# Kernel optimization log

Hardware: AMD Instinct MI355X
Metric: run time of the kernel (lower is better)

## Reference

```python
import jax, jax.numpy as jnp
import numpy as np

N_QUBITS = 6
DIM = 2 ** N_QUBITS  # 64


def _b(t, nd):
    # broadcast a (B,) per-sample angle factor (or scalar) against a state slice of rank nd
    if jnp.ndim(t) == 0:
        return t
    return t.reshape((t.shape[0],) + (1,) * (nd - 1))


def _ry(state, theta, q):
    ax = q + 1
    s0 = jnp.take(state, 0, axis=ax)
    s1 = jnp.take(state, 1, axis=ax)
    h = theta * 0.5
    c = _b(jnp.cos(h), s0.ndim)
    s = _b(jnp.sin(h), s0.ndim)
    return jnp.stack([c * s0 - s * s1, s * s0 + c * s1], axis=ax)


def _rx(state, theta, q):
    ax = q + 1
    s0 = jnp.take(state, 0, axis=ax)
    s1 = jnp.take(state, 1, axis=ax)
    h = theta * 0.5
    c = _b(jnp.cos(h), s0.ndim)
    s = _b(jnp.sin(h), s0.ndim)
    return jnp.stack([c * s0 - 1j * s * s1, -1j * s * s0 + c * s1], axis=ax)


def _rz(state, theta, q):
    ax = q + 1
    s0 = jnp.take(state, 0, axis=ax)
    s1 = jnp.take(state, 1, axis=ax)
    h = theta * 0.5
    p0 = _b(jnp.exp(-1j * h), s0.ndim)
    p1 = _b(jnp.exp(1j * h), s0.ndim)
    return jnp.stack([p0 * s0, p1 * s1], axis=ax)


def _cnot(state, ctrl, tgt):
    ca = ctrl + 1
    s0 = jnp.take(state, 0, axis=ca)
    s1 = jnp.take(state, 1, axis=ca)
    ta = tgt + 1 if tgt < ctrl else tgt  # target axis after removing control axis
    s1 = jnp.flip(s1, axis=ta)
    return jnp.stack([s0, s1], axis=ca)


def quantum_circuit(inputs, weights):
    # inputs: (B, 6) float; weights: (5, 6) float -> (B, 6) PauliZ expectations
    B = inputs.shape[0]
    scaled = jnp.clip(inputs, -1.0, 1.0) * jnp.pi
    state = jnp.zeros((B,) + (2,) * N_QUBITS, dtype=jnp.complex64)
    state = state.at[(slice(None),) + (0,) * N_QUBITS].set(1.0)
    for i in range(N_QUBITS):
        state = _ry(state, scaled[:, i], i)
    for i in range(N_QUBITS):
        state = _rx(state, weights[0, i], i)
        state = _rz(state, weights[1, i], i)
    for i in range(N_QUBITS - 1):
        state = _cnot(state, i, i + 1)
    state = _cnot(state, N_QUBITS - 1, 0)
    for i in range(N_QUBITS):
        state = _ry(state, weights[2, i], i)
        state = _rz(state, weights[3, i], i)
    for i in range(0, N_QUBITS, 2):
        state = _cnot(state, i, (i + 1) % N_QUBITS)
    for i in range(N_QUBITS):
        state = _rx(state, weights[4, i], i)
    probs = (state.real ** 2 + state.imag ** 2).reshape(B, DIM)
    # Z eigenvalue table: qubit q is bit (5-q) of the flat index
    k = jnp.arange(DIM)
    z = (1 - 2 * ((k[None, :] >> (N_QUBITS - 1 - jnp.arange(N_QUBITS)[:, None])) & 1)).astype(jnp.float32)
    return probs @ z.T  # (B, 6)


def setup_inputs() -> dict:
    key = jax.random.key(0)
    ks = jax.random.split(key, 13)
    B, n_symptoms, n_dep, nq = 262144, 128, 20, N_QUBITS

    def lin(k, fi, fo):
        bound = 1.0 / np.sqrt(fi)
        kw, kb = jax.random.split(k)
        W = jax.random.uniform(kw, (fi, fo), jnp.float32, -bound, bound)
        b = jax.random.uniform(kb, (fo,), jnp.float32, -bound, bound)
        return W, b

    x = jax.random.normal(ks[0], (B, n_symptoms), jnp.float32)
    W1, b1 = lin(ks[1], n_symptoms, 32)
    W2, b2 = lin(ks[2], 32, 16)
    W3, b3 = lin(ks[3], 16, nq)
    qw = jax.random.normal(ks[4], (5, nq), jnp.float32)
    W4, b4 = lin(ks[5], nq, 16)
    W5, b5 = lin(ks[6], 16, n_dep)
    return {"x": x, "W1": W1, "b1": b1, "W2": W2, "b2": b2, "W3": W3, "b3": b3,
            "qw": qw, "W4": W4, "b4": b4, "W5": W5, "b5": b5}


def reference(x, W1, b1, W2, b2, W3, b3, qw, W4, b4, W5, b5):
    h = jax.nn.relu(x @ W1 + b1)            # Dropout(0.2) is identity at eval
    h = jax.nn.relu(h @ W2 + b2)
    pre = jnp.tanh(h @ W3 + b3)             # (B, 6)
    # Original detaches before the quantum circuit -> stop_gradient for fidelity
    q_out = quantum_circuit(jax.lax.stop_gradient(pre), jax.lax.stop_gradient(qw))
    h = jax.nn.relu(q_out @ W4 + b4)
    return h @ W5 + b5                      # (B, n_departments)
```

## Files before the change

### kernel.cpp

```cpp
#include <hip/hip_runtime.h>
#include <hip/hip_bf16.h>
#include <math.h>

#define PI_F 3.14159265358979323846f

typedef float f32x4 __attribute__((ext_vector_type(4)));
typedef short bf16x8 __attribute__((ext_vector_type(8)));

__device__ __forceinline__ unsigned short bf_hi(float f) {
    return (unsigned short)(__float_as_uint(f) >> 16);
}
__device__ __forceinline__ float from_bf(unsigned short h) {
    return __uint_as_float(((unsigned)h) << 16);
}

__global__ __launch_bounds__(64) void build_u(const float* __restrict__ qw,
                                              float* __restrict__ Umat) {
    const int l = threadIdx.x;
    const int b = blockIdx.x;

    float ar = (l == b) ? 1.0f : 0.0f;
    float ai = 0.0f;

    #pragma unroll
    for (int i = 0; i < 6; ++i) {
        const int mask = 1 << (5 - i);
        float th = 0.5f * qw[0 * 6 + i];
        float c = cosf(th), sn = sinf(th);
        float pr = __shfl_xor(ar, mask);
        float pi = __shfl_xor(ai, mask);
        float nr = c * ar + sn * pi;
        float ni = c * ai - sn * pr;
        ar = nr; ai = ni;
        th = 0.5f * qw[1 * 6 + i];
        c = cosf(th); sn = sinf(th);
        float zn = (l & mask) ? 1.0f : -1.0f;
        nr = c * ar - zn * sn * ai;
        ni = c * ai + zn * sn * ar;
        ar = nr; ai = ni;
    }

    #pragma unroll
    for (int i = 0; i < 6; ++i) {
        const int ctrl = i, tgt = (i + 1) % 6;
        const int cm = 1 << (5 - ctrl), tm = 1 << (5 - tgt);
        float pr = __shfl_xor(ar, tm);
        float pi = __shfl_xor(ai, tm);
        bool take = (l & cm) != 0;
        ar = take ? pr : ar;
        ai = take ? pi : ai;
    }

    #pragma unroll
    for (int i = 0; i < 6; ++i) {
        const int mask = 1 << (5 - i);
        float th = 0.5f * qw[2 * 6 + i];
        float c = cosf(th), sn = sinf(th);
        float pr = __shfl_xor(ar, mask);
        float pi = __shfl_xor(ai, mask);
        float sg = (l & mask) ? sn : -sn;
        float nr = c * ar + sg * pr;
        float ni = c * ai + sg * pi;
        ar = nr; ai = ni;
        th = 0.5f * qw[3 * 6 + i];
        c = cosf(th); sn = sinf(th);
        float zn = (l & mask) ? 1.0f : -1.0f;
        nr = c * ar - zn * sn * ai;
        ni = c * ai + zn * sn * ar;
        ar = nr; ai = ni;
    }

    #pragma unroll
    for (int i = 0; i < 6; i += 2) {
        const int cm = 1 << (5 - i), tm = 1 << (5 - (i + 1));
        float pr = __shfl_xor(ar, tm);
        float pi = __shfl_xor(ai, tm);
        bool take = (l & cm) != 0;
        ar = take ? pr : ar;
        ai = take ? pi : ai;
    }

    #pragma unroll
    for (int i = 0; i < 6; ++i) {
        const int mask = 1 << (5 - i);
        float th = 0.5f * qw[4 * 6 + i];
        float c = cosf(th), sn = sinf(th);
        float pr = __shfl_xor(ar, mask);
        float pi = __shfl_xor(ai, mask);
        float nr = c * ar + sn * pi;
        float ni = c * ai - sn * pr;
        ar = nr; ai = ni;
    }

    Umat[(l * 64 + b) * 2 + 0] = ar;
    Umat[(l * 64 + b) * 2 + 1] = ai;
}

__global__ __launch_bounds__(64) void convert_u(const float* __restrict__ Umat,
                                                unsigned short* __restrict__ Ubf) {
    const int l = threadIdx.x;
    bf16x8* out8 = reinterpret_cast<bf16x8*>(Ubf);

    #pragma unroll
    for (int ri = 0; ri < 2; ++ri) {
        #pragma unroll
        for (int t = 0; t < 4; ++t) {
            #pragma unroll
            for (int h = 0; h < 2; ++h) {
                const int vf = (ri * 4 + t) * 2 + h;
                bf16x8 vh, vl;
                #pragma unroll
                for (int e = 0; e < 8; ++e) {
                    const int k = 16 * t + (l & 15);
                    const int j = h * 32 + (l >> 4) * 8 + e;
                    float v = Umat[k * 128 + j * 2 + ri];
                    unsigned short hh = bf_hi(v);
                    float rem = v - from_bf(hh);
                    unsigned short ll = bf_hi(rem);
                    vh[e] = (short)hh;
                    vl[e] = (short)ll;
                }
                out8[(vf * 2 + 0) * 64 + l] = vh;
                out8[(vf * 2 + 1) * 64 + l] = vl;
            }
        }
    }
}

__device__ __forceinline__ void front_tail(
    const float h1[32],
    const float* __restrict__ W2, const float* __restrict__ b2,
    const float* __restrict__ W3, const float* __restrict__ b3,
    float lo[8], float hi[8])
{
    float h2[16];
    #pragma unroll
    for (int o = 0; o < 16; ++o) h2[o] = b2[o];
    #pragma unroll
    for (int j = 0; j < 32; ++j) {
        #pragma unroll
        for (int o = 0; o < 16; ++o) h2[o] = fmaf(h1[j], W2[j * 16 + o], h2[o]);
    }
    #pragma unroll
    for (int o = 0; o < 16; ++o) h2[o] = fmaxf(h2[o], 0.0f);

    float cq[6], sq[6];
    #pragma unroll
    for (int q = 0; q < 6; ++q) {
        float t = b3[q];
        #pragma unroll
        for (int j = 0; j < 16; ++j) t = fmaf(h2[j], W3[j * 6 + q], t);
        t = tanhf(t);
        t = fminf(1.0f, fmaxf(-1.0f, t));
        float half = t * (0.5f * PI_F);
        sq[q] = sinf(half);
        cq[q] = cosf(half);
    }

    {
        float f3[2] = {cq[3], sq[3]};
        float f4[2] = {cq[4], sq[4]};
        float f5[2] = {cq[5], sq[5]};
        #pragma unroll
        for (int m = 0; m < 8; ++m)
            lo[m] = f3[(m >> 2) & 1] * f4[(m >> 1) & 1] * f5[m & 1];
        float f0[2] = {cq[0], sq[0]};
        float f1[2] = {cq[1], sq[1]};
        float f2[2] = {cq[2], sq[2]};
        #pragma unroll
        for (int m = 0; m < 8; ++m)
            hi[m] = f0[(m >> 2) & 1] * f1[(m >> 1) & 1] * f2[m & 1];
    }
}

__global__ __launch_bounds__(256) void front_kernel(
    const float* __restrict__ x,
    const float* __restrict__ W1, const float* __restrict__ b1,
    const float* __restrict__ W2, const float* __restrict__ b2,
    const float* __restrict__ W3, const float* __restrict__ b3,
    float* __restrict__ tab, int B)
{
    __shared__ float Ls[256 * 36];

    const int tid = threadIdx.x;
    const long sbase = (long)blockIdx.x * 256;
    const int s = (int)(sbase + tid);

    const f32x4* xg = reinterpret_cast<const f32x4*>(x);

    float h1[32];
    #pragma unroll
    for (int o = 0; o < 32; ++o) h1[o] = b1[o];

    #pragma unroll 1
    for (int tile = 0; tile < 4; ++tile) {
        #pragma unroll
        for (int i = 0; i < 8; ++i) {
            const int flat = i * 256 + tid;
            const int row = flat >> 3;
            const int c4  = flat & 7;
            long srow = sbase + row;
            if (srow >= B) srow = B - 1;
            f32x4 v = __builtin_nontemporal_load(&xg[(size_t)srow * 32 + tile * 8 + c4]);
            *reinterpret_cast<f32x4*>(&Ls[row * 36 + c4 * 4]) = v;
        }
        __syncthreads();

        #pragma unroll
        for (int c4 = 0; c4 < 8; ++c4) {
            float4 xv = *reinterpret_cast<const float4*>(&Ls[tid * 36 + c4 * 4]);
            const float* w = W1 + (tile * 32 + c4 * 4) * 32;
            #pragma unroll
            for (int o = 0; o < 32; ++o) h1[o] = fmaf(xv.x, w[o], h1[o]);
            #pragma unroll
            for (int o = 0; o < 32; ++o) h1[o] = fmaf(xv.y, w[32 + o], h1[o]);
            #pragma unroll
            for (int o = 0; o < 32; ++o) h1[o] = fmaf(xv.z, w[64 + o], h1[o]);
            #pragma unroll
            for (int o = 0; o < 32; ++o) h1[o] = fmaf(xv.w, w[96 + o], h1[o]);
        }
        __syncthreads();
    }

    #pragma unroll
    for (int o = 0; o < 32; ++o) h1[o] = fmaxf(h1[o], 0.0f);

    float lo[8], hi[8];
    front_tail(h1, W2, b2, W3, b3, lo, hi);

    if (s < B) {
        #pragma unroll
        for (int i = 0; i < 8; ++i)
            __builtin_nontemporal_store(lo[i], &tab[(size_t)i * B + s]);
        #pragma unroll
        for (int i = 0; i < 8; ++i)
            __builtin_nontemporal_store(hi[i], &tab[(size_t)(8 + i) * B + s]);
    }
}

__global__ __launch_bounds__(256) void gemv_mfma(
    const float* __restrict__ tab,
    const unsigned short* __restrict__ Ubf,
    const float* __restrict__ W4, const float* __restrict__ b4,
    const float* __restrict__ W5, const float* __restrict__ b5,
    float* __restrict__ out, int B)
{
    __shared__ float qlds[64][8];

    const int tid  = threadIdx.x;
    const int wv   = tid >> 6;
    const int lane = tid & 63;
    const int g    = lane >> 4;
    const int c    = lane & 15;
    const long blk = (long)blockIdx.x * 64;
    const int s    = (int)(blk + wv * 16 + c);
    const int s_ld = (s < B) ? s : (B - 1);

    float tl[8], th[8];
    #pragma unroll
    for (int i = 0; i < 8; ++i)
        tl[i] = __builtin_nontemporal_load(&tab[(size_t)i * B + s_ld]);
    #pragma unroll
    for (int i = 0; i < 8; ++i)
        th[i] = __builtin_nontemporal_load(&tab[(size_t)(8 + i) * B + s_ld]);

    float bh0 = (g == 0) ? th[0] : (g == 1) ? th[1] : (g == 2) ? th[2] : th[3];
    float bh1 = (g == 0) ? th[4] : (g == 1) ? th[5] : (g == 2) ? th[6] : th[7];

    bf16x8 Ah0, Al0, Ah1, Al1;
    #pragma unroll
    for (int e = 0; e < 8; ++e) {
        float p0 = bh0 * tl[e];
        unsigned short h0 = bf_hi(p0);
        Ah0[e] = (short)h0;
        Al0[e] = (short)bf_hi(p0 - from_bf(h0));
        float p1 = bh1 * tl[e];
        unsigned short h1 = bf_hi(p1);
        Ah1[e] = (short)h1;
        Al1[e] = (short)bf_hi(p1 - from_bf(h1));
    }

    const bf16x8* Ub = reinterpret_cast<const bf16x8*>(Ubf);

    f32x4 accre[4], accim[4];
    #pragma unroll
    for (int t = 0; t < 4; ++t) { accre[t] = (f32x4)0.0f; accim[t] = (f32x4)0.0f; }

    #pragma unroll
    for (int t = 0; t < 4; ++t) {
        bf16x8 B0h = Ub[(((0 * 4 + t) * 2 + 0) * 2 + 0) * 64 + lane];
        bf16x8 B0l = Ub[(((0 * 4 + t) * 2 + 0) * 2 + 1) * 64 + lane];
        bf16x8 B1h = Ub[(((0 * 4 + t) * 2 + 1) * 2 + 0) * 64 + lane];
        bf16x8 B1l = Ub[(((0 * 4 + t) * 2 + 1) * 2 + 1) * 64 + lane];
        accre[t] = __builtin_amdgcn_mfma_f32_16x16x32_bf16(Ah0, B0h, accre[t], 0, 0, 0);
        accre[t] = __builtin_amdgcn_mfma_f32_16x16x32_bf16(Al0, B0h, accre[t], 0, 0, 0);
        accre[t] = __builtin_amdgcn_mfma_f32_16x16x32_bf16(Ah0, B0l, accre[t], 0, 0, 0);
        accre[t] = __builtin_amdgcn_mfma_f32_16x16x32_bf16(Ah1, B1h, accre[t], 0, 0, 0);
        accre[t] = __builtin_amdgcn_mfma_f32_16x16x32_bf16(Al1, B1h, accre[t], 0, 0, 0);
        accre[t] = __builtin_amdgcn_mfma_f32_16x16x32_bf16(Ah1, B1l, accre[t], 0, 0, 0);
    }
    #pragma unroll
    for (int t = 0; t < 4; ++t) {
        bf16x8 B0h = Ub[(((1 * 4 + t) * 2 + 0) * 2 + 0) * 64 + lane];
        bf16x8 B0l = Ub[(((1 * 4 + t) * 2 + 0) * 2 + 1) * 64 + lane];
        bf16x8 B1h = Ub[(((1 * 4 + t) * 2 + 1) * 2 + 0) * 64 + lane];
        bf16x8 B1l = Ub[(((1 * 4 + t) * 2 + 1) * 2 + 1) * 64 + lane];
        accim[t] = __builtin_amdgcn_mfma_f32_16x16x32_bf16(Ah0, B0h, accim[t], 0, 0, 0);
        accim[t] = __builtin_amdgcn_mfma_f32_16x16x32_bf16(Al0, B0h, accim[t], 0, 0, 0);
        accim[t] = __builtin_amdgcn_mfma_f32_16x16x32_bf16(Ah0, B0l, accim[t], 0, 0, 0);
        accim[t] = __builtin_amdgcn_mfma_f32_16x16x32_bf16(Ah1, B1h, accim[t], 0, 0, 0);
        accim[t] = __builtin_amdgcn_mfma_f32_16x16x32_bf16(Al1, B1h, accim[t], 0, 0, 0);
        accim[t] = __builtin_amdgcn_mfma_f32_16x16x32_bf16(Ah1, B1l, accim[t], 0, 0, 0);
    }

    #pragma unroll
    for (int r = 0; r < 4; ++r) {
        float p0 = accre[0][r] * accre[0][r] + accim[0][r] * accim[0][r];
        float p1 = accre[1][r] * accre[1][r] + accim[1][r] * accim[1][r];
        float p2 = accre[2][r] * accre[2][r] + accim[2][r] * accim[2][r];
        float p3 = accre[3][r] * accre[3][r] + accim[3][r] * accim[3][r];

        float P0 = p0 + p1 + p2 + p3;
        float P1 = p0 + p1 - p2 - p3;
        float P2 = p0 - p1 + p2 - p3;

        float v = P0;
        #pragma unroll
        for (int st = 0; st < 4; ++st) {
            const int m = 1 << st;
            float prt = __shfl_xor(v, m);
            v = (lane & m) ? (prt - v) : (prt + v);
        }
        #pragma unroll
        for (int st = 0; st < 4; ++st) P1 += __shfl_xor(P1, 1 << st);
        #pragma unroll
        for (int st = 0; st < 4; ++st) P2 += __shfl_xor(P2, 1 << st);

        const int sl = wv * 16 + g * 4 + r;
        if (c == 0) { qlds[sl][0] = P1; qlds[sl][1] = P2; }
        if (c == 8) qlds[sl][2] = v;
        if (c == 4) qlds[sl][3] = v;
        if (c == 2) qlds[sl][4] = v;
        if (c == 1) qlds[sl][5] = v;
    }

    __syncthreads();

    if (tid < 64) {
        const int so = (int)(blk + tid);
        if (so < B) {
            float qv[6];
            #pragma unroll
            for (int i = 0; i < 6; ++i) qv[i] = qlds[tid][i];

            float h4[16];
            #pragma unroll
            for (int o = 0; o < 16; ++o) h4[o] = b4[o];
            #pragma unroll
            for (int q = 0; q < 6; ++q) {
                #pragma unroll
                for (int o = 0; o < 16; ++o) h4[o] = fmaf(qv[q], W4[q * 16 + o], h4[o]);
            }
            #pragma unroll
            for (int o = 0; o < 16; ++o) h4[o] = fmaxf(h4[o], 0.0f);

            float o5[20];
            #pragma unroll
            for (int o = 0; o < 20; ++o) {
                float t = b5[o];
                #pragma unroll
                for (int j = 0; j < 16; ++j) t = fmaf(h4[j], W5[j * 20 + o], t);
                o5[o] = t;
            }

            f32x4* outv = reinterpret_cast<f32x4*>(out + (size_t)so * 20);
            #pragma unroll
            for (int i = 0; i < 5; ++i) {
                f32x4 v = {o5[4 * i], o5[4 * i + 1], o5[4 * i + 2], o5[4 * i + 3]};
                __builtin_nontemporal_store(v, &outv[i]);
            }
        }
    }
}

extern "C" void kernel_launch(void* const* d_in, const int* in_sizes, int n_in,
                              void* d_out, int out_size, void* d_ws, size_t ws_size,
                              hipStream_t stream) {
    const float* x  = (const float*)d_in[0];
    const float* W1 = (const float*)d_in[1];
    const float* b1 = (const float*)d_in[2];
    const float* W2 = (const float*)d_in[3];
    const float* b2 = (const float*)d_in[4];
    const float* W3 = (const float*)d_in[5];
    const float* b3 = (const float*)d_in[6];
    const float* qw = (const float*)d_in[7];
    const float* W4 = (const float*)d_in[8];
    const float* b4 = (const float*)d_in[9];
    const float* W5 = (const float*)d_in[10];
    const float* b5 = (const float*)d_in[11];
    float* out = (float*)d_out;

    const int B = in_sizes[0] / 128;

    float* Umat = (float*)d_ws;
    unsigned short* Ubf = (unsigned short*)((float*)d_ws + 8192);
    float* tab  = (float*)d_ws + 16384;

    build_u<<<64, 64, 0, stream>>>(qw, Umat);
    convert_u<<<1, 64, 0, stream>>>(Umat, Ubf);
    front_kernel<<<(B + 255) / 256, 256, 0, stream>>>(
        x, W1, b1, W2, b2, W3, b3, tab, B);
    gemv_mfma<<<(B + 63) / 64, 256, 0, stream>>>(
        tab, Ubf, W4, b4, W5, b5, out, B);
}
```

Measured before the change: 106.5 us.

## Move first MLP layer onto bf16x3 split MFMA with pre-split weights

The first linear layer (128->32) in the front kernel moves from per-thread scalar FMAs to MFMA 16x16x32 bf16 instructions. Inputs and W1 are split into high and low bf16 parts, and three products are accumulated to approximate fp32 precision. W1 is pre-split once in the merged conversion kernel. Results go through LDS so each thread can run the rest of the MLP on its sample. This cuts VALU FMA work and weight reloads, at the cost of a slight precision change, an extra LDS round trip, and uncoalesced per-row global loads of x.

```diff
diff --git a/kernel.cpp b/kernel.cpp
--- a/kernel.cpp
+++ b/kernel.cpp
@@ -96,8 +96,10 @@
     Umat[(l * 64 + b) * 2 + 1] = ai;
 }
 
-__global__ __launch_bounds__(64) void convert_u(const float* __restrict__ Umat,
-                                                unsigned short* __restrict__ Ubf) {
+__global__ __launch_bounds__(64) void convert_all(
+    const float* __restrict__ Umat, const float* __restrict__ W1,
+    unsigned short* __restrict__ Ubf, unsigned short* __restrict__ W1bf)
+{
     const int l = threadIdx.x;
     bf16x8* out8 = reinterpret_cast<bf16x8*>(Ubf);
 
@@ -115,14 +117,30 @@
                     const int j = h * 32 + (l >> 4) * 8 + e;
                     float v = Umat[k * 128 + j * 2 + ri];
                     unsigned short hh = bf_hi(v);
-                    float rem = v - from_bf(hh);
-                    unsigned short ll = bf_hi(rem);
                     vh[e] = (short)hh;
-                    vl[e] = (short)ll;
+                    vl[e] = (short)bf_hi(v - from_bf(hh));
                 }
                 out8[(vf * 2 + 0) * 64 + l] = vh;
                 out8[(vf * 2 + 1) * 64 + l] = vl;
             }
+        }
+    }
+
+    bf16x8* w8 = reinterpret_cast<bf16x8*>(W1bf);
+    #pragma unroll
+    for (int ks = 0; ks < 4; ++ks) {
+        #pragma unroll
+        for (int nt = 0; nt < 2; ++nt) {
+            bf16x8 vh, vl;
+            #pragma unroll
+            for (int e = 0; e < 8; ++e) {
+                float v = W1[(ks * 32 + (l >> 4) * 8 + e) * 32 + nt * 16 + (l & 15)];
+                unsigned short hh = bf_hi(v);
+                vh[e] = (short)hh;
+                vl[e] = (short)bf_hi(v - from_bf(hh));
+            }
+            w8[((ks * 2 + nt) * 2 + 0) * 64 + l] = vh;
+            w8[((ks * 2 + nt) * 2 + 1) * 64 + l] = vl;
         }
     }
 }
@@ -173,57 +191,78 @@
     }
 }
 
-__global__ __launch_bounds__(256) void front_kernel(
+__global__ __launch_bounds__(256) void front_mfma(
     const float* __restrict__ x,
-    const float* __restrict__ W1, const float* __restrict__ b1,
+    const unsigned short* __restrict__ W1bf, const float* __restrict__ b1,
     const float* __restrict__ W2, const float* __restrict__ b2,
     const float* __restrict__ W3, const float* __restrict__ b3,
     float* __restrict__ tab, int B)
 {
-    __shared__ float Ls[256 * 36];
-
-    const int tid = threadIdx.x;
-    const long sbase = (long)blockIdx.x * 256;
-    const int s = (int)(sbase + tid);
-
-    const f32x4* xg = reinterpret_cast<const f32x4*>(x);
-
+    __shared__ float h1lds[256][33];
+
+    const int tid  = threadIdx.x;
+    const int wv   = tid >> 6;
+    const int lane = tid & 63;
+    const int g    = lane >> 4;
+    const int c    = lane & 15;
+    const long blk = (long)blockIdx.x * 256;
+
+    const bf16x8* Wb = reinterpret_cast<const bf16x8*>(W1bf);
+
+    #pragma unroll
+    for (int mt = 0; mt < 4; ++mt) {
+        long t0 = blk + wv * 64 + mt * 16 + c;
+        const int srow = (int)((t0 < B) ? t0 : (B - 1));
+        const float* xrow = x + (size_t)srow * 128;
+
+        f32x4 acc0 = (f32x4)0.0f, acc1 = (f32x4)0.0f;
+
+        #pragma unroll
+        for (int ks = 0; ks < 4; ++ks) {
+            f32x4 xa = __builtin_nontemporal_load(
+                reinterpret_cast<const f32x4*>(xrow + ks * 32 + g * 8));
+            f32x4 xb = __builtin_nontemporal_load(
+                reinterpret_cast<const f32x4*>(xrow + ks * 32 + g * 8 + 4));
+            bf16x8 Ah, Al;
+            #pragma unroll
+            for (int e = 0; e < 4; ++e) {
+                unsigned short hh = bf_hi(xa[e]);
+                Ah[e] = (short)hh;
+                Al[e] = (short)bf_hi(xa[e] - from_bf(hh));
+            }
+            #pragma unroll
+            for (int e = 0; e < 4; ++e) {
+                unsigned short hh = bf_hi(xb[e]);
+                Ah[4 + e] = (short)hh;
+                Al[4 + e] = (short)bf_hi(xb[e] - from_bf(hh));
+            }
+
+            bf16x8 B0h = Wb[((ks * 2 + 0) * 2 + 0) * 64 + lane];
+            bf16x8 B0l = Wb[((ks * 2 + 0) * 2 + 1) * 64 + lane];
+            bf16x8 B1h = Wb[((ks * 2 + 1) * 2 + 0) * 64 + lane];
+            bf16x8 B1l = Wb[((ks * 2 + 1) * 2 + 1) * 64 + lane];
+
+            acc0 = __builtin_amdgcn_mfma_f32_16x16x32_bf16(Ah, B0h, acc0, 0, 0, 0);
+            acc0 = __builtin_amdgcn_mfma_f32_16x16x32_bf16(Al, B0h, acc0, 0, 0, 0);
+            acc0 = __builtin_amdgcn_mfma_f32_16x16x32_bf16(Ah, B0l, acc0, 0, 0, 0);
+            acc1 = __builtin_amdgcn_mfma_f32_16x16x32_bf16(Ah, B1h, acc1, 0, 0, 0);
+            acc1 = __builtin_amdgcn_mfma_f32_16x16x32_bf16(Al, B1h, acc1, 0, 0, 0);
+            acc1 = __builtin_amdgcn_mfma_f32_16x16x32_bf16(Ah, B1l, acc1, 0, 0, 0);
+        }
+
+        #pragma unroll
+        for (int r = 0; r < 4; ++r) {
+            h1lds[wv * 64 + mt * 16 + g * 4 + r][c]      = acc0[r];
+            h1lds[wv * 64 + mt * 16 + g * 4 + r][16 + c] = acc1[r];
+        }
+    }
+
+    __syncthreads();
+
+    const int s = (int)(blk + tid);
     float h1[32];
     #pragma unroll
-    for (int o = 0; o < 32; ++o) h1[o] = b1[o];
-
-    #pragma unroll 1
-    for (int tile = 0; tile < 4; ++tile) {
-        #pragma unroll
-        for (int i = 0; i < 8; ++i) {
-            const int flat = i * 256 + tid;
-            const int row = flat >> 3;
-            const int c4  = flat & 7;
-            long srow = sbase + row;
-            if (srow >= B) srow = B - 1;
-            f32x4 v = __builtin_nontemporal_load(&xg[(size_t)srow * 32 + tile * 8 + c4]);
-            *reinterpret_cast<f32x4*>(&Ls[row * 36 + c4 * 4]) = v;
-        }
-        __syncthreads();
-
-        #pragma unroll
-        for (int c4 = 0; c4 < 8; ++c4) {
-            float4 xv = *reinterpret_cast<const float4*>(&Ls[tid * 36 + c4 * 4]);
-            const float* w = W1 + (tile * 32 + c4 * 4) * 32;
-            #pragma unroll
-            for (int o = 0; o < 32; ++o) h1[o] = fmaf(xv.x, w[o], h1[o]);
-            #pragma unroll
-            for (int o = 0; o < 32; ++o) h1[o] = fmaf(xv.y, w[32 + o], h1[o]);
-            #pragma unroll
-            for (int o = 0; o < 32; ++o) h1[o] = fmaf(xv.z, w[64 + o], h1[o]);
-            #pragma unroll
-            for (int o = 0; o < 32; ++o) h1[o] = fmaf(xv.w, w[96 + o], h1[o]);
-        }
-        __syncthreads();
-    }
-
-    #pragma unroll
-    for (int o = 0; o < 32; ++o) h1[o] = fmaxf(h1[o], 0.0f);
+    for (int o = 0; o < 32; ++o) h1[o] = fmaxf(h1lds[tid][o] + b1[o], 0.0f);
 
     float lo[8], hi[8];
     front_tail(h1, W2, b2, W3, b3, lo, hi);
@@ -403,13 +442,14 @@
     const int B = in_sizes[0] / 128;
 
     float* Umat = (float*)d_ws;
-    unsigned short* Ubf = (unsigned short*)((float*)d_ws + 8192);
-    float* tab  = (float*)d_ws + 16384;
+    unsigned short* Ubf  = (unsigned short*)((float*)d_ws + 8192);
+    unsigned short* W1bf = (unsigned short*)((float*)d_ws + 16384);
+    float* tab  = (float*)d_ws + 20480;
 
     build_u<<<64, 64, 0, stream>>>(qw, Umat);
-    convert_u<<<1, 64, 0, stream>>>(Umat, Ubf);
-    front_kernel<<<(B + 255) / 256, 256, 0, stream>>>(
-        x, W1, b1, W2, b2, W3, b3, tab, B);
+    convert_all<<<1, 64, 0, stream>>>(Umat, W1, Ubf, W1bf);
+    front_mfma<<<(B + 255) / 256, 256, 0, stream>>>(
+        x, W1bf, b1, W2, b2, W3, b3, tab, B);
     gemv_mfma<<<(B + 63) / 64, 256, 0, stream>>>(
         tab, Ubf, W4, b4, W5, b5, out, B);
 }
```

Measured after the change: 101.3 us. -4.9%, faster.
